# Performance work log

Measured on AMD Instinct MI355X. Metric: run time of the kernel, lower is better.

Reference implementation:

```python
import jax, jax.numpy as jnp
import numpy as np

N = 50000      # nodes
E = 800000     # edges (avg degree 16)
NR = 32        # relation types
D_IN = 128
D_OUT = 128
EPS = 1e-5     # BatchNorm eps


def setup_inputs() -> dict:
    key = jax.random.key(0)
    ks = jax.random.split(key, 8)
    xav = (2.0 / (D_IN + D_OUT)) ** 0.5  # xavier_normal std
    return {
        "node_feat": jax.random.normal(ks[0], (N, D_IN), jnp.float32),
        "edge_feat": jax.random.normal(ks[1], (NR, D_IN), jnp.float32),
        "W_R": jax.random.normal(ks[2], (NR, D_IN, D_OUT), jnp.float32) * xav,
        "W_rel": jax.random.normal(ks[3], (D_IN, D_OUT), jnp.float32) * xav,
        "bn_gamma": jnp.ones((D_OUT,), jnp.float32),
        "bn_beta": jnp.zeros((D_OUT,), jnp.float32),
        "etype_norm": jax.random.uniform(ks[4], (E,), jnp.float32),
        "src": jax.random.randint(ks[5], (E,), 0, N),
        "dst": jax.random.randint(ks[6], (E,), 0, N),
        "etype": jax.random.randint(ks[7], (E,), 0, NR),
    }


def reference(node_feat, edge_feat, W_R, W_rel, bn_gamma, bn_beta,
              etype_norm, src, dst, etype):
    # comp: elementwise 'mult' composition of src node feat with relation embedding
    # scaled by per-edge norm (norm-scale commutes with the linear W_R matmul).
    comp = node_feat[src] * edge_feat[etype] * etype_norm[:, None]  # [E, D_IN]
    # Aggregate composed messages per (relation, dst-node) BEFORE the per-relation
    # matmul (valid since sum-aggregation and matmul are linear) -> avoids [E,D,D].
    seg = etype * N + dst
    agg = jax.ops.segment_sum(comp, seg, num_segments=NR * N)       # [NR*N, D_IN]
    agg = agg.reshape(NR, N, D_IN)
    h = jnp.einsum('rnd,rdo->no', agg, W_R)                         # [N, D_OUT]
    # dropout p=0.0 -> identity. BatchNorm1d (training-mode batch stats, biased var).
    mean = jnp.mean(h, axis=0)
    var = jnp.mean(jnp.square(h - mean), axis=0)
    h = (h - mean) * jax.lax.rsqrt(var + EPS) * bn_gamma + bn_beta
    return jnp.tanh(h), edge_feat @ W_rel
```

## Files before the change

### kernel.cpp

```cpp
#include <hip/hip_runtime.h>
#include <cstdint>
#include <cstddef>

#define NN 50000
#define NE 800000
#define NREL 32
#define DIM 128
#define BN_EPS 1e-5f
#define WTE 16

#define WS_H      0
#define WS_WMOD   6400000
#define WS_SNORM  6924288
#define WS_SSRC   7724288
#define WS_SDST   8524288
#define WS_CNT    9324288
#define WS_OFF    9324320
#define WS_CURSOR 9324353
#define WS_STATS  9324385
#define WS_END    9324641

__global__ void k_wmod(const float* __restrict__ ef, const float* __restrict__ WR,
                       float* __restrict__ wmod) {
    int idx = blockIdx.x * 256 + threadIdx.x;
    int r = idx >> 14;
    int d = (idx >> 7) & 127;
    wmod[idx] = ef[(r << 7) + d] * WR[idx];
}

__global__ void k_hist(const int* __restrict__ etype, int* __restrict__ cnt) {
    __shared__ int lc[NREL];
    if (threadIdx.x < NREL) lc[threadIdx.x] = 0;
    __syncthreads();
    for (int i = blockIdx.x * blockDim.x + threadIdx.x; i < NE;
         i += gridDim.x * blockDim.x)
        atomicAdd(&lc[etype[i]], 1);
    __syncthreads();
    if (threadIdx.x < NREL) atomicAdd(&cnt[threadIdx.x], lc[threadIdx.x]);
}

__global__ void k_scan(const int* __restrict__ cnt, int* __restrict__ off,
                       int* __restrict__ cursor) {
    if (threadIdx.x == 0) {
        int a = 0;
        for (int r = 0; r < NREL; ++r) {
            off[r] = a; cursor[r] = a; a += cnt[r];
        }
        off[NREL] = a;
    }
}

__global__ void k_scatter(const int* __restrict__ etype, const int* __restrict__ src,
                          const int* __restrict__ dst, const float* __restrict__ norm,
                          int* __restrict__ cursor,
                          int* __restrict__ ssrc, int* __restrict__ sdst,
                          float* __restrict__ snorm) {
    __shared__ int lc[NREL], lbase[NREL];
    int i0 = blockIdx.x * 2048;
    int i1 = min(i0 + 2048, NE);
    if (threadIdx.x < NREL) lc[threadIdx.x] = 0;
    __syncthreads();
    for (int i = i0 + threadIdx.x; i < i1; i += 256)
        atomicAdd(&lc[etype[i]], 1);
    __syncthreads();
    if (threadIdx.x < NREL) {
        lbase[threadIdx.x] = atomicAdd(&cursor[threadIdx.x], lc[threadIdx.x]);
        lc[threadIdx.x] = 0;
    }
    __syncthreads();
    for (int i = i0 + threadIdx.x; i < i1; i += 256) {
        int et = etype[i];
        int pos = lbase[et] + atomicAdd(&lc[et], 1);
        ssrc[pos] = src[i];
        sdst[pos] = dst[i];
        snorm[pos] = norm[i];
    }
}

__global__ void k_out2(const float* __restrict__ ef, const float* __restrict__ wrel,
                       float* __restrict__ out2) {
    int r = blockIdx.x;
    int o = threadIdx.x;
    float y0 = 0.f, y1 = 0.f;
    #pragma unroll
    for (int d = 0; d < DIM; d += 2) {
        y0 = fmaf(ef[r * DIM + d],     wrel[d * DIM + o],       y0);
        y1 = fmaf(ef[r * DIM + d + 1], wrel[(d + 1) * DIM + o], y1);
    }
    out2[r * DIM + o] = y0 + y1;
}

__global__ __launch_bounds__(512, 2)
void k_gemm(const float* __restrict__ node_feat, const float* __restrict__ wmod,
            const int* __restrict__ ssrc, const int* __restrict__ sdst,
            const float* __restrict__ snorm, const int* __restrict__ off,
            float* __restrict__ h) {
    __shared__ float Ws[DIM][DIM];
    __shared__ float Xw[8][DIM][WTE];
    const int t = threadIdx.x;
    const int r  = blockIdx.x >> 3;
    const int bq = blockIdx.x & 7;

    {
        const float* wsrc = wmod + ((size_t)r << 14);
        float* wdst = &Ws[0][0];
        #pragma unroll
        for (int i = 0; i < 8; ++i) {
            int idx = i * 2048 + t * 4;
            *(float4*)&wdst[idx] = *(const float4*)&wsrc[idx];
        }
    }
    __syncthreads();

    const int wv = t >> 6;
    const int l  = t & 63;
    float (*Xs)[WTE] = Xw[wv];
    const int seg  = l >> 4;
    const int srow = l & 15;
    const int cm = l >> 4;
    const int cn = l & 15;

    const int beg_r = off[r], end_r = off[r + 1];
    const int cnt_r = end_r - beg_r;
    const int Lb = (cnt_r + 7) >> 3;
    const int b0 = beg_r + bq * Lb;
    const int b1 = min(b0 + Lb, end_r);
    const int span = b1 > b0 ? b1 - b0 : 0;
    const int Lw = (span + 7) >> 3;
    const int s0 = b0 + wv * Lw;
    const int s1 = min(s0 + Lw, b1);

    for (int tb = s0; tb < s1; tb += WTE) {
        const int cnt_t = min(WTE, s1 - tb);

        int   se = 0;
        float nm = 0.f;
        if (srow < cnt_t) { se = ssrc[tb + srow]; nm = snorm[tb + srow]; }
        const float* xp = node_feat + ((size_t)se << 7);
        #pragma unroll
        for (int i = 0; i < 8; ++i) {
            int d0 = i * 16 + seg * 4;
            float4 v = *(const float4*)&xp[d0];
            Xs[d0][srow]     = v.x * nm;
            Xs[d0 + 1][srow] = v.y * nm;
            Xs[d0 + 2][srow] = v.z * nm;
            Xs[d0 + 3][srow] = v.w * nm;
        }
        __builtin_amdgcn_wave_barrier();

        float acc[4][8];
        #pragma unroll
        for (int a = 0; a < 4; ++a)
            #pragma unroll
            for (int cc = 0; cc < 8; ++cc) acc[a][cc] = 0.f;

        #pragma unroll 8
        for (int k = 0; k < DIM; ++k) {
            float4 xf = *(const float4*)&Xs[k][cm * 4];
            float4 wa = *(const float4*)&Ws[k][cn * 4];
            float4 wb = *(const float4*)&Ws[k][64 + cn * 4];
            const float xv[4] = {xf.x, xf.y, xf.z, xf.w};
            const float wv8[8] = {wa.x, wa.y, wa.z, wa.w, wb.x, wb.y, wb.z, wb.w};
            #pragma unroll
            for (int a = 0; a < 4; ++a)
                #pragma unroll
                for (int cc = 0; cc < 8; ++cc)
                    acc[a][cc] = fmaf(xv[a], wv8[cc], acc[a][cc]);
        }
        __builtin_amdgcn_wave_barrier();

        float* O = &Xs[0][0];
        #pragma unroll
        for (int a = 0; a < 4; ++a) {
            int row = cm * 4 + a;
            *(float4*)&O[row * DIM + cn * 4] =
                make_float4(acc[a][0], acc[a][1], acc[a][2], acc[a][3]);
            *(float4*)&O[row * DIM + 64 + cn * 4] =
                make_float4(acc[a][4], acc[a][5], acc[a][6], acc[a][7]);
        }
        __builtin_amdgcn_wave_barrier();

        #pragma unroll
        for (int rr = 0; rr < WTE; ++rr) {
            if (rr < cnt_t) {
                int d2 = sdst[tb + rr];
                float* hp = h + ((size_t)d2 << 7);
                atomicAdd(&hp[l],      O[rr * DIM + l]);
                atomicAdd(&hp[64 + l], O[rr * DIM + 64 + l]);
            }
        }
        __builtin_amdgcn_wave_barrier();
    }
}

__global__ void k_bnstat(const float* __restrict__ h, float* __restrict__ stats) {
    const int t = threadIdx.x;
    const int o = t & 127;
    const int half = t >> 7;
    float s = 0.f, ss = 0.f;
    for (int n = blockIdx.x * 2 + half; n < NN; n += gridDim.x * 2) {
        float v = h[(size_t)n * DIM + o];
        s += v; ss += v * v;
    }
    __shared__ float bs[256], bss[256];
    bs[t] = s; bss[t] = ss;
    __syncthreads();
    if (t < 128) {
        atomicAdd(&stats[o],       bs[t] + bs[t + 128]);
        atomicAdd(&stats[128 + o], bss[t] + bss[t + 128]);
    }
}

__global__ void k_bnapply(const float* __restrict__ h, const float* __restrict__ stats,
                          const float* __restrict__ gamma, const float* __restrict__ beta,
                          float* __restrict__ out) {
    const float invN = 1.f / (float)NN;
    for (int idx = blockIdx.x * 256 + threadIdx.x; idx < NN * DIM;
         idx += gridDim.x * 256) {
        int o = idx & 127;
        float mean = stats[o] * invN;
        float var  = stats[128 + o] * invN - mean * mean;
        float v = (h[idx] - mean) * rsqrtf(var + BN_EPS) * gamma[o] + beta[o];
        out[idx] = tanhf(v);
    }
}

extern "C" void kernel_launch(void* const* d_in, const int* in_sizes, int n_in,
                              void* d_out, int out_size, void* d_ws, size_t ws_size,
                              hipStream_t stream) {
    const float* node_feat = (const float*)d_in[0];
    const float* edge_feat = (const float*)d_in[1];
    const float* W_R       = (const float*)d_in[2];
    const float* W_rel     = (const float*)d_in[3];
    const float* bn_gamma  = (const float*)d_in[4];
    const float* bn_beta   = (const float*)d_in[5];
    const float* enorm     = (const float*)d_in[6];
    const int*   src       = (const int*)d_in[7];
    const int*   dst       = (const int*)d_in[8];
    const int*   etype     = (const int*)d_in[9];

    float* ws_f = (float*)d_ws;
    int*   ws_i = (int*)d_ws;

    float* h      = ws_f + WS_H;
    float* wmod   = ws_f + WS_WMOD;
    float* snorm  = ws_f + WS_SNORM;
    int*   ssrc   = ws_i + WS_SSRC;
    int*   sdst   = ws_i + WS_SDST;
    int*   cnt    = ws_i + WS_CNT;
    int*   off    = ws_i + WS_OFF;
    int*   cursor = ws_i + WS_CURSOR;
    float* stats  = ws_f + WS_STATS;

    float* out_h  = (float*)d_out;
    float* out2   = (float*)d_out + NN * DIM;

    hipMemsetAsync(h, 0, (size_t)NN * DIM * sizeof(float), stream);
    hipMemsetAsync(ws_i + WS_CNT, 0, (WS_END - WS_CNT) * sizeof(int), stream);

    k_wmod    <<<2048, 256, 0, stream>>>(edge_feat, W_R, wmod);
    k_hist    <<<256, 256, 0, stream>>>(etype, cnt);
    k_scan    <<<1, 64, 0, stream>>>(cnt, off, cursor);
    k_scatter <<<(NE + 2047) / 2048, 256, 0, stream>>>(etype, src, dst, enorm,
                                                       cursor, ssrc, sdst, snorm);
    k_out2    <<<NREL, DIM, 0, stream>>>(edge_feat, W_rel, out2);
    k_gemm    <<<NREL * 8, 512, 0, stream>>>(node_feat, wmod, ssrc, sdst,
                                             snorm, off, h);
    k_bnstat  <<<512, 256, 0, stream>>>(h, stats);
    k_bnapply <<<2048, 256, 0, stream>>>(h, stats, bn_gamma, bn_beta, out_h);
}
```

Before: 584.2 us.

## Use split-bf16 MFMA for per-relation GEMM and fuse prep kernels

Replaces the FP32 scalar FMA GEMM in k_gemm with bf16 MFMA 16x16x32 instructions. Both operands are split into hi and lo bf16 parts and three products are accumulated to keep near-FP32 accuracy. W is prearranged into a fragment layout in a new k_prep kernel, which also absorbs the wmod, histogram and out2 kernels. The h zeroing memset moves into k_scatter, and LDS output staging uses a rotated index to avoid bank conflicts. The per-edge atomic scatter into h is unchanged and may still dominate, and the split precision adds conversion work and slightly different rounding.

```diff
diff --git a/kernel.cpp b/kernel.cpp
--- a/kernel.cpp
+++ b/kernel.cpp
@@ -10,7 +10,7 @@
 #define WTE 16
 
 #define WS_H      0
-#define WS_WMOD   6400000
+#define WS_WFRAG  6400000
 #define WS_SNORM  6924288
 #define WS_SSRC   7724288
 #define WS_SDST   8524288
@@ -20,23 +20,56 @@
 #define WS_STATS  9324385
 #define WS_END    9324641
 
-__global__ void k_wmod(const float* __restrict__ ef, const float* __restrict__ WR,
-                       float* __restrict__ wmod) {
-    int idx = blockIdx.x * 256 + threadIdx.x;
-    int r = idx >> 14;
-    int d = (idx >> 7) & 127;
-    wmod[idx] = ef[(r << 7) + d] * WR[idx];
-}
-
-__global__ void k_hist(const int* __restrict__ etype, int* __restrict__ cnt) {
-    __shared__ int lc[NREL];
-    if (threadIdx.x < NREL) lc[threadIdx.x] = 0;
-    __syncthreads();
-    for (int i = blockIdx.x * blockDim.x + threadIdx.x; i < NE;
-         i += gridDim.x * blockDim.x)
-        atomicAdd(&lc[etype[i]], 1);
-    __syncthreads();
-    if (threadIdx.x < NREL) atomicAdd(&cnt[threadIdx.x], lc[threadIdx.x]);
+typedef __attribute__((ext_vector_type(8))) short bf16x8;
+typedef __attribute__((ext_vector_type(4))) float f32x4;
+typedef __attribute__((ext_vector_type(8))) unsigned short ush8;
+
+__device__ __forceinline__ unsigned short f2bf(float f) {
+    unsigned int u = __float_as_uint(f);
+    return (unsigned short)((u + 0x7fffu + ((u >> 16) & 1u)) >> 16);
+}
+__device__ __forceinline__ float bf2f(unsigned short b) {
+    return __uint_as_float(((unsigned int)b) << 16);
+}
+
+__global__ void k_prep(const float* __restrict__ ef, const float* __restrict__ WR,
+                       const float* __restrict__ wrel, const int* __restrict__ etype,
+                       unsigned short* __restrict__ whi, unsigned short* __restrict__ wlo,
+                       float* __restrict__ out2, int* __restrict__ cnt) {
+    int b = blockIdx.x;
+    if (b < 2048) {
+        int idx = b * 256 + threadIdx.x;
+        int r = idx >> 14, k = (idx >> 7) & 127, n = idx & 127;
+        float w = ef[(r << 7) + k] * WR[idx];
+        unsigned short hi = f2bf(w);
+        unsigned short lo = f2bf(w - bf2f(hi));
+        int kc = k >> 5, j = k & 7;
+        int lane = (((k >> 3) & 3) << 4) | (n & 15);
+        int nc = n >> 4;
+        int off = (r << 14) + (((((kc << 3) + nc) << 6) + lane) << 3) + j;
+        whi[off] = hi;
+        wlo[off] = lo;
+    } else if (b < 2080) {
+        int r = b - 2048;
+        int o = threadIdx.x;
+        if (o < DIM) {
+            float y0 = 0.f, y1 = 0.f;
+            #pragma unroll
+            for (int d = 0; d < DIM; d += 2) {
+                y0 = fmaf(ef[r * DIM + d],     wrel[d * DIM + o],       y0);
+                y1 = fmaf(ef[r * DIM + d + 1], wrel[(d + 1) * DIM + o], y1);
+            }
+            out2[r * DIM + o] = y0 + y1;
+        }
+    } else {
+        __shared__ int lc[NREL];
+        if (threadIdx.x < NREL) lc[threadIdx.x] = 0;
+        __syncthreads();
+        for (int i = (b - 2080) * 256 + threadIdx.x; i < NE; i += 64 * 256)
+            atomicAdd(&lc[etype[i]], 1);
+        __syncthreads();
+        if (threadIdx.x < NREL) atomicAdd(&cnt[threadIdx.x], lc[threadIdx.x]);
+    }
 }
 
 __global__ void k_scan(const int* __restrict__ cnt, int* __restrict__ off,
@@ -54,7 +87,12 @@
                           const int* __restrict__ dst, const float* __restrict__ norm,
                           int* __restrict__ cursor,
                           int* __restrict__ ssrc, int* __restrict__ sdst,
-                          float* __restrict__ snorm) {
+                          float* __restrict__ snorm, float* __restrict__ hbuf) {
+    float4 z4 = make_float4(0.f, 0.f, 0.f, 0.f);
+    for (int i = blockIdx.x * 256 + threadIdx.x; i < NN * DIM / 4;
+         i += gridDim.x * 256)
+        ((float4*)hbuf)[i] = z4;
+
     __shared__ int lc[NREL], lbase[NREL];
     int i0 = blockIdx.x * 2048;
     int i1 = min(i0 + 2048, NE);
@@ -77,48 +115,36 @@
     }
 }
 
-__global__ void k_out2(const float* __restrict__ ef, const float* __restrict__ wrel,
-                       float* __restrict__ out2) {
-    int r = blockIdx.x;
-    int o = threadIdx.x;
-    float y0 = 0.f, y1 = 0.f;
-    #pragma unroll
-    for (int d = 0; d < DIM; d += 2) {
-        y0 = fmaf(ef[r * DIM + d],     wrel[d * DIM + o],       y0);
-        y1 = fmaf(ef[r * DIM + d + 1], wrel[(d + 1) * DIM + o], y1);
-    }
-    out2[r * DIM + o] = y0 + y1;
-}
-
 __global__ __launch_bounds__(512, 2)
-void k_gemm(const float* __restrict__ node_feat, const float* __restrict__ wmod,
+void k_gemm(const float* __restrict__ node_feat,
+            const unsigned short* __restrict__ whi,
+            const unsigned short* __restrict__ wlo,
             const int* __restrict__ ssrc, const int* __restrict__ sdst,
             const float* __restrict__ snorm, const int* __restrict__ off,
             float* __restrict__ h) {
-    __shared__ float Ws[DIM][DIM];
-    __shared__ float Xw[8][DIM][WTE];
+    __shared__ unsigned short WfHi[16384], WfLo[16384];
+    __shared__ float Os[8][WTE * DIM];
     const int t = threadIdx.x;
     const int r  = blockIdx.x >> 3;
     const int bq = blockIdx.x & 7;
 
     {
-        const float* wsrc = wmod + ((size_t)r << 14);
-        float* wdst = &Ws[0][0];
-        #pragma unroll
-        for (int i = 0; i < 8; ++i) {
-            int idx = i * 2048 + t * 4;
-            *(float4*)&wdst[idx] = *(const float4*)&wsrc[idx];
+        const unsigned short* gh = whi + (r << 14);
+        const unsigned short* gl = wlo + (r << 14);
+        #pragma unroll
+        for (int i = 0; i < 4; ++i) {
+            int idx = i * 4096 + t * 8;
+            *(ush8*)&WfHi[idx] = *(const ush8*)&gh[idx];
+            *(ush8*)&WfLo[idx] = *(const ush8*)&gl[idx];
         }
     }
     __syncthreads();
 
     const int wv = t >> 6;
     const int l  = t & 63;
-    float (*Xs)[WTE] = Xw[wv];
-    const int seg  = l >> 4;
-    const int srow = l & 15;
-    const int cm = l >> 4;
-    const int cn = l & 15;
+    const int er = l & 15;
+    const int kg = l >> 4;
+    float* O = Os[wv];
 
     const int beg_r = off[r], end_r = off[r + 1];
     const int cnt_r = end_r - beg_r;
@@ -135,48 +161,47 @@
 
         int   se = 0;
         float nm = 0.f;
-        if (srow < cnt_t) { se = ssrc[tb + srow]; nm = snorm[tb + srow]; }
-        const float* xp = node_feat + ((size_t)se << 7);
-        #pragma unroll
-        for (int i = 0; i < 8; ++i) {
-            int d0 = i * 16 + seg * 4;
-            float4 v = *(const float4*)&xp[d0];
-            Xs[d0][srow]     = v.x * nm;
-            Xs[d0 + 1][srow] = v.y * nm;
-            Xs[d0 + 2][srow] = v.z * nm;
-            Xs[d0 + 3][srow] = v.w * nm;
+        if (er < cnt_t) { se = ssrc[tb + er]; nm = snorm[tb + er]; }
+        const float* xp = node_feat + ((size_t)se << 7) + kg * 8;
+
+        f32x4 acc[8];
+        const f32x4 zero4 = {0.f, 0.f, 0.f, 0.f};
+        #pragma unroll
+        for (int nc = 0; nc < 8; ++nc) acc[nc] = zero4;
+
+        #pragma unroll
+        for (int kc = 0; kc < 4; ++kc) {
+            float4 x0 = *(const float4*)&xp[kc * 32];
+            float4 x1 = *(const float4*)&xp[kc * 32 + 4];
+            float xs[8] = {x0.x * nm, x0.y * nm, x0.z * nm, x0.w * nm,
+                           x1.x * nm, x1.y * nm, x1.z * nm, x1.w * nm};
+            bf16x8 ah, al;
+            #pragma unroll
+            for (int j = 0; j < 8; ++j) {
+                unsigned short hb = f2bf(xs[j]);
+                ah[j] = (short)hb;
+                al[j] = (short)f2bf(xs[j] - bf2f(hb));
+            }
+            #pragma unroll
+            for (int nc = 0; nc < 8; ++nc) {
+                int boff = ((((kc << 3) + nc) << 6) + l) << 3;
+                bf16x8 bh = *(const bf16x8*)&WfHi[boff];
+                bf16x8 bl = *(const bf16x8*)&WfLo[boff];
+                acc[nc] = __builtin_amdgcn_mfma_f32_16x16x32_bf16(ah, bh, acc[nc], 0, 0, 0);
+                acc[nc] = __builtin_amdgcn_mfma_f32_16x16x32_bf16(al, bh, acc[nc], 0, 0, 0);
+                acc[nc] = __builtin_amdgcn_mfma_f32_16x16x32_bf16(ah, bl, acc[nc], 0, 0, 0);
+            }
         }
         __builtin_amdgcn_wave_barrier();
 
-        float acc[4][8];
-        #pragma unroll
-        for (int a = 0; a < 4; ++a)
-            #pragma unroll
-            for (int cc = 0; cc < 8; ++cc) acc[a][cc] = 0.f;
-
-        #pragma unroll 8
-        for (int k = 0; k < DIM; ++k) {
-            float4 xf = *(const float4*)&Xs[k][cm * 4];
-            float4 wa = *(const float4*)&Ws[k][cn * 4];
-            float4 wb = *(const float4*)&Ws[k][64 + cn * 4];
-            const float xv[4] = {xf.x, xf.y, xf.z, xf.w};
-            const float wv8[8] = {wa.x, wa.y, wa.z, wa.w, wb.x, wb.y, wb.z, wb.w};
-            #pragma unroll
-            for (int a = 0; a < 4; ++a)
-                #pragma unroll
-                for (int cc = 0; cc < 8; ++cc)
-                    acc[a][cc] = fmaf(xv[a], wv8[cc], acc[a][cc]);
-        }
-        __builtin_amdgcn_wave_barrier();
-
-        float* O = &Xs[0][0];
-        #pragma unroll
-        for (int a = 0; a < 4; ++a) {
-            int row = cm * 4 + a;
-            *(float4*)&O[row * DIM + cn * 4] =
-                make_float4(acc[a][0], acc[a][1], acc[a][2], acc[a][3]);
-            *(float4*)&O[row * DIM + 64 + cn * 4] =
-                make_float4(acc[a][4], acc[a][5], acc[a][6], acc[a][7]);
+        #pragma unroll
+        for (int nc = 0; nc < 8; ++nc) {
+            #pragma unroll
+            for (int q = 0; q < 4; ++q) {
+                int row = kg * 4 + q;
+                int c = nc * 16 + er;
+                O[row * DIM + ((c + 2 * row) & 127)] = acc[nc][q];
+            }
         }
         __builtin_amdgcn_wave_barrier();
 
@@ -185,8 +210,8 @@
             if (rr < cnt_t) {
                 int d2 = sdst[tb + rr];
                 float* hp = h + ((size_t)d2 << 7);
-                atomicAdd(&hp[l],      O[rr * DIM + l]);
-                atomicAdd(&hp[64 + l], O[rr * DIM + 64 + l]);
+                atomicAdd(&hp[l],      O[rr * DIM + ((l + 2 * rr) & 127)]);
+                atomicAdd(&hp[64 + l], O[rr * DIM + ((64 + l + 2 * rr) & 127)]);
             }
         }
         __builtin_amdgcn_wave_barrier();
@@ -242,29 +267,28 @@
     float* ws_f = (float*)d_ws;
     int*   ws_i = (int*)d_ws;
 
-    float* h      = ws_f + WS_H;
-    float* wmod   = ws_f + WS_WMOD;
-    float* snorm  = ws_f + WS_SNORM;
-    int*   ssrc   = ws_i + WS_SSRC;
-    int*   sdst   = ws_i + WS_SDST;
-    int*   cnt    = ws_i + WS_CNT;
-    int*   off    = ws_i + WS_OFF;
-    int*   cursor = ws_i + WS_CURSOR;
-    float* stats  = ws_f + WS_STATS;
+    float*          h      = ws_f + WS_H;
+    unsigned short* whi    = (unsigned short*)(ws_f + WS_WFRAG);
+    unsigned short* wlo    = whi + NREL * 16384;
+    float*          snorm  = ws_f + WS_SNORM;
+    int*            ssrc   = ws_i + WS_SSRC;
+    int*            sdst   = ws_i + WS_SDST;
+    int*            cnt    = ws_i + WS_CNT;
+    int*            off    = ws_i + WS_OFF;
+    int*            cursor = ws_i + WS_CURSOR;
+    float*          stats  = ws_f + WS_STATS;
 
     float* out_h  = (float*)d_out;
     float* out2   = (float*)d_out + NN * DIM;
 
-    hipMemsetAsync(h, 0, (size_t)NN * DIM * sizeof(float), stream);
     hipMemsetAsync(ws_i + WS_CNT, 0, (WS_END - WS_CNT) * sizeof(int), stream);
 
-    k_wmod    <<<2048, 256, 0, stream>>>(edge_feat, W_R, wmod);
-    k_hist    <<<256, 256, 0, stream>>>(etype, cnt);
+    k_prep    <<<2144, 256, 0, stream>>>(edge_feat, W_R, W_rel, etype,
+                                         whi, wlo, out2, cnt);
     k_scan    <<<1, 64, 0, stream>>>(cnt, off, cursor);
     k_scatter <<<(NE + 2047) / 2048, 256, 0, stream>>>(etype, src, dst, enorm,
-                                                       cursor, ssrc, sdst, snorm);
-    k_out2    <<<NREL, DIM, 0, stream>>>(edge_feat, W_rel, out2);
-    k_gemm    <<<NREL * 8, 512, 0, stream>>>(node_feat, wmod, ssrc, sdst,
+                                                       cursor, ssrc, sdst, snorm, h);
+    k_gemm    <<<NREL * 8, 512, 0, stream>>>(node_feat, whi, wlo, ssrc, sdst,
                                              snorm, off, h);
     k_bnstat  <<<512, 256, 0, stream>>>(h, stats);
     k_bnapply <<<2048, 256, 0, stream>>>(h, stats, bn_gamma, bn_beta, out_h);
```

New measurement: 531.5 us. -9.0%, faster.
